# Performance work log

Hardware: AMD Instinct MI355X
Metric: run time of the kernel (lower is better)

Reference implementation:

```python
import jax, jax.numpy as jnp
import numpy as np

TAU = 1.0
K_TAU = 1.0
MAX_K = 64


def setup_inputs() -> dict:
    key = jax.random.key(0)
    ks = jax.random.split(key, 6)
    B, S, D, H = 8, 4096, 1024, 2048
    token_embeddings = jax.random.normal(ks[0], (B, S, D), dtype=jnp.float32)
    W1 = jax.random.normal(ks[1], (D, H), dtype=jnp.float32) * (1.0 / np.sqrt(D))
    b1 = jnp.zeros((H,), dtype=jnp.float32)
    W2 = jax.random.normal(ks[2], (H, 1), dtype=jnp.float32) * (1.0 / np.sqrt(H))
    b2 = jnp.zeros((1,), dtype=jnp.float32)
    k_logits = jax.random.normal(ks[3], (MAX_K,), dtype=jnp.float32) * 0.02
    return {"token_embeddings": token_embeddings, "W1": W1, "b1": b1,
            "W2": W2, "b2": b2, "k_logits": k_logits}


def _gumbel(rng, shape):
    u = jax.random.uniform(rng, shape, minval=1e-08, maxval=1.0 - 1e-08)
    return -jnp.log(-jnp.log(u))


def reference(token_embeddings, W1, b1, W2, b2, k_logits):
    B, S, D = token_embeddings.shape
    # scorer: Dense -> relu -> Dense(1), squeeze -> [B, S]
    h = jax.nn.relu(jnp.einsum('bsd,dh->bsh', token_embeddings, W1) + b1)
    importance_logits = (jnp.einsum('bsh,ho->bso', h, W2) + b2)[..., 0]

    rng = jax.random.key(42)  # training rng
    rng1, rng2 = jax.random.split(rng)

    # learnable-k selection (training branch)
    k_gumbel = _gumbel(rng1, k_logits.shape)
    k_soft = jax.nn.softmax((k_logits + k_gumbel) / K_TAU)
    expected_k = jnp.sum(k_soft * jnp.arange(1, MAX_K + 1, dtype=k_soft.dtype))
    k_selected = jnp.argmax(k_soft) + 1  # traced int scalar

    # gumbel-softmax hard top-k over tokens
    perturbed = importance_logits + _gumbel(rng2, importance_logits.shape)
    soft_mask = jax.nn.softmax(perturbed / TAU, axis=-1)  # [B, S]
    # rank of each token (0 = smallest); top-k == rank >= S - k
    rank = jnp.argsort(jnp.argsort(soft_mask, axis=-1), axis=-1)
    hard_mask = (rank >= S - k_selected).astype(soft_mask.dtype)
    selection_mask = jax.lax.stop_gradient(hard_mask - soft_mask) + soft_mask

    filtered_embeddings = token_embeddings * selection_mask[..., None]
    return filtered_embeddings, selection_mask, expected_k
```

## Files before the change

kernel.cpp:

```cpp
#include <hip/hip_runtime.h>
#include <stdint.h>

#define B_BATCH 8
#define S_SEQ   4096
#define D_DIM   1024
#define H_DIM   2048
#define M_TOK   (B_BATCH * S_SEQ)
#define MAXK    64
#define NSPLIT  2

typedef unsigned int u32;
typedef unsigned short u16;
typedef unsigned long long u64;
typedef __attribute__((ext_vector_type(8))) short short8;
typedef __attribute__((ext_vector_type(4))) float f32x4;

#define GLOBAL_AS __attribute__((address_space(1)))
#define LDS_AS    __attribute__((address_space(3)))


#define TF_ROUND(x0, x1, r) { x0 += x1; x1 = ((x1 << r) | (x1 >> (32 - r))); x1 ^= x0; }

__device__ __forceinline__ void tf2x32(u32 k0, u32 k1, u32 x0, u32 x1, u32& o0, u32& o1) {
  u32 k2 = k0 ^ k1 ^ 0x1BD11BDAu;
  x0 += k0; x1 += k1;
  TF_ROUND(x0, x1, 13) TF_ROUND(x0, x1, 15) TF_ROUND(x0, x1, 26) TF_ROUND(x0, x1, 6)
  x0 += k1; x1 += k2 + 1u;
  TF_ROUND(x0, x1, 17) TF_ROUND(x0, x1, 29) TF_ROUND(x0, x1, 16) TF_ROUND(x0, x1, 24)
  x0 += k2; x1 += k0 + 2u;
  TF_ROUND(x0, x1, 13) TF_ROUND(x0, x1, 15) TF_ROUND(x0, x1, 26) TF_ROUND(x0, x1, 6)
  x0 += k0; x1 += k1 + 3u;
  TF_ROUND(x0, x1, 17) TF_ROUND(x0, x1, 29) TF_ROUND(x0, x1, 16) TF_ROUND(x0, x1, 24)
  x0 += k1; x1 += k2 + 4u;
  TF_ROUND(x0, x1, 13) TF_ROUND(x0, x1, 15) TF_ROUND(x0, x1, 26) TF_ROUND(x0, x1, 6)
  x0 += k2; x1 += k0 + 5u;
  o0 = x0; o1 = x1;
}

__device__ __forceinline__ void jax_subkeys(u32& r1a, u32& r1b, u32& r2a, u32& r2b) {
  tf2x32(0u, 42u, 0u, 0u, r1a, r1b);
  tf2x32(0u, 42u, 0u, 1u, r2a, r2b);
}

__device__ __forceinline__ u32 jax_bits32(u32 ka, u32 kb, u32 i) {
  u32 o0, o1;
  tf2x32(ka, kb, 0u, i, o0, o1);
  return o0 ^ o1;
}

__device__ __forceinline__ float jax_uniform_from_bits(u32 bits) {
  float f = __uint_as_float((bits >> 9) | 0x3f800000u) - 1.0f;
  float r = f + 1e-8f;
  return fmaxf(1e-8f, r);
}

__device__ __forceinline__ float gumbel_from_bits(u32 bits) {
  float u = jax_uniform_from_bits(bits);
  return -logf(-logf(u));
}

__device__ __forceinline__ u32 ordf(float v) {
  u32 b = __float_as_uint(v);
  return (b & 0x80000000u) ? ~b : (b | 0x80000000u);
}

__device__ __forceinline__ u64 shflx64(u64 v, int m) {
  unsigned lo = (unsigned)v, hi = (unsigned)(v >> 32);
  lo = (unsigned)__shfl_xor((int)lo, m);
  hi = (unsigned)__shfl_xor((int)hi, m);
  return ((u64)hi << 32) | lo;
}


__device__ __forceinline__ u16 f2bf_rn(float x) {
  u32 u = __float_as_uint(x);
  u32 r = u + 0x7fffu + ((u >> 16) & 1u);
  return (u16)(r >> 16);
}

__device__ __forceinline__ void split1(float x, u16& h, u16& lo) {
  h = f2bf_rn(x);
  float hf = __uint_as_float(((u32)h) << 16);
  lo = f2bf_rn(x - hf);
}


__global__ __launch_bounds__(256) void prep_a_img(const float* __restrict__ x,
                                                  u16* __restrict__ img) {
  const u32 t = blockIdx.x * 256 + threadIdx.x;
  const int idx512 = (int)(t & 511);
  const int u1 = (int)((t >> 9) & 1);
  const int kt = (int)((t >> 10) & 31);
  const int mt = (int)(t >> 15);
  const int w = idx512 >> 6, l = idx512 & 63;
  const int sig = w * 16 + (l >> 2);
  const int r = sig + (sig & 64) + u1 * 64;
  const int c = (l & 3) ^ ((sig >> 1) & 3);
  const float* src = x + (size_t)(mt * 256 + r) * D_DIM + kt * 32 + c * 8;
  float4 v0 = *(const float4*)src;
  float4 v1 = *(const float4*)(src + 4);
  union { u16 a[8]; short8 v; } H, L;
  split1(v0.x, H.a[0], L.a[0]); split1(v0.y, H.a[1], L.a[1]);
  split1(v0.z, H.a[2], L.a[2]); split1(v0.w, H.a[3], L.a[3]);
  split1(v1.x, H.a[4], L.a[4]); split1(v1.y, H.a[5], L.a[5]);
  split1(v1.z, H.a[6], L.a[6]); split1(v1.w, H.a[7], L.a[7]);
  u16* dhi = img + (size_t)(mt * 32 + kt) * 16384 + u1 * 4096 + idx512 * 8;
  *(short8*)dhi = H.v;
  *(short8*)(dhi + 8192) = L.v;
}

__global__ __launch_bounds__(256) void prep_b_img(const float* __restrict__ W1,
                                                  u16* __restrict__ img) {
  __shared__ float tile[64][33];
  const int tid = threadIdx.x;
  const int bid = blockIdx.x;
  const int n0 = (bid & 63) * 32, k0 = (bid >> 6) * 64;
  const int tx = tid & 31, ty = tid >> 5;
  #pragma unroll
  for (int rr = 0; rr < 8; ++rr)
    tile[ty + rr * 8][tx] = W1[(size_t)(k0 + ty + rr * 8) * H_DIM + n0 + tx];
  __syncthreads();
  const int nc = tid & 31, c8 = tid >> 5;
  const int ktl = c8 >> 2, cc = c8 & 3;
  const int n = n0 + nc;
  const int nyb = n >> 10, t8 = (n >> 8) & 3, rr_ = n & 255;
  const int hiU = rr_ >> 7;
  const int sig = rr_ & 127;
  const int w_ = sig >> 4;
  const int lpos = (sig & 15) * 4 + (cc ^ ((sig >> 1) & 3));
  const int kt = (k0 >> 5) + ktl;
  union { u16 a[8]; short8 v; } H, L;
  #pragma unroll
  for (int j = 0; j < 8; ++j)
    split1(tile[ktl * 32 + cc * 8 + j][nc], H.a[j], L.a[j]);
  u16* d = img + (size_t)nyb * 2097152 + (size_t)(t8 * 32 + kt) * 16384
               + hiU * 4096 + w_ * 512 + lpos * 8;
  *(short8*)d = H.v;
  *(short8*)(d + 8192) = L.v;
}


__device__ __forceinline__ void stage16(const u16* g, u16* l) {
  __builtin_amdgcn_global_load_lds((const GLOBAL_AS u32*)g, (LDS_AS u32*)l, 16, 0, 0);
}

#define WAITV(N) asm volatile("s_waitcnt vmcnt(" #N ")" ::: "memory")
#define FENCE()  asm volatile("" ::: "memory")

__global__ __launch_bounds__(512, 2) void scorer_mfma256(
    const u16* __restrict__ Aimg, const u16* __restrict__ Bimg,
    const float* __restrict__ b1, const float* __restrict__ W2,
    float* __restrict__ pl) {
  extern __shared__ u16 smem[];
  float* red = (float*)(smem + 65536);

  const int tid = threadIdx.x;
  const int w = tid >> 6, l = tid & 63;
  const int wm = w >> 2, wn = w & 3;

  const int b = blockIdx.x;
  const int xcd = b & 7;
  const int j = b >> 3;
  const int nyb = j & 1;
  const int mt = xcd * 16 + (j >> 1);
  const int m0 = mt * 256;

  const u16* const Amt = Aimg + (size_t)mt * 524288;
  const u16* const Bny = Bimg + (size_t)nyb * 2097152;
  const int lane16 = w * 512 + l * 8;
  u16* const ldsw = smem + w * 512;

#define ST_A(T, U) stage16(Amt + (size_t)((((T) & 31) * 16384) + (U) * 4096) + lane16, \
                           ldsw + (((T) & 1) << 15) + (U) * 4096)
#define ST_B(T, U) stage16(Bny + (size_t)(((((T) >> 5) * 32 + ((T) & 31)) * 16384) + (U) * 4096) + lane16, \
                           ldsw + (((T) & 1) << 15) + 16384 + (U) * 4096)

  int a_off[8], b_off[4];
  #pragma unroll
  for (int mf = 0; mf < 8; ++mf) {
    int slot = wm * 64 + (mf & 3) * 16 + (l & 15);
    a_off[mf] = ((mf >> 2) * 4096) + slot * 32 + (((l >> 4) ^ ((slot >> 1) & 3)) << 3);
  }
  #pragma unroll
  for (int nf = 0; nf < 4; ++nf) {
    int r = wn * 64 + nf * 16 + (l & 15);
    b_off[nf] = r * 32 + (((l >> 4) ^ ((r >> 1) & 3)) << 3);
  }

  f32x4 acc[8][4];
  #pragma unroll
  for (int mf = 0; mf < 8; ++mf)
    #pragma unroll
    for (int nf = 0; nf < 4; ++nf) acc[mf][nf] = (f32x4){0.f, 0.f, 0.f, 0.f};

  const u16* const B0 = smem;
  const u16* const B1 = smem + 32768;
  short8 ah[4], al[4], bh[4], bl[4];

#define LDA_E(BASE) \
  { _Pragma("unroll") \
    for (int i = 0; i < 4; ++i) { \
      ah[i] = *(const short8*)((BASE) + a_off[i]); \
      al[i] = *(const short8*)((BASE) + 8192 + a_off[i]); \
    } }

#define LDA_L(BASE) \
  { _Pragma("unroll") \
    for (int i = 0; i < 4; ++i) { \
      ah[i] = *(const short8*)((BASE) + a_off[4 + i]); \
      al[i] = *(const short8*)((BASE) + 8192 + a_off[4 + i]); \
    } }

#define LDB(BASE) \
  { _Pragma("unroll") \
    for (int nf = 0; nf < 4; ++nf) { \
      bh[nf] = *(const short8*)((BASE) + 16384 + b_off[nf]); \
      bl[nf] = *(const short8*)((BASE) + 24576 + b_off[nf]); \
    } }

#define MMA_QUAD(MB) \
  __builtin_amdgcn_s_setprio(1); \
  { _Pragma("unroll") \
    for (int mf = 0; mf < 4; ++mf) \
      _Pragma("unroll") \
      for (int nf = 0; nf < 4; ++nf) { \
        acc[(MB) + mf][nf] = __builtin_amdgcn_mfma_f32_16x16x32_bf16(ah[mf], bh[nf], acc[(MB) + mf][nf], 0, 0, 0); \
        acc[(MB) + mf][nf] = __builtin_amdgcn_mfma_f32_16x16x32_bf16(ah[mf], bl[nf], acc[(MB) + mf][nf], 0, 0, 0); \
        acc[(MB) + mf][nf] = __builtin_amdgcn_mfma_f32_16x16x32_bf16(al[mf], bh[nf], acc[(MB) + mf][nf], 0, 0, 0); \
      } } \
  __builtin_amdgcn_s_setprio(0)

  ST_B(0, 0); ST_B(0, 1); ST_B(0, 2); ST_B(0, 3);
  ST_A(0, 0); ST_A(0, 2);
  ST_A(0, 1); ST_A(0, 3);
  ST_B(1, 0); ST_B(1, 1); ST_B(1, 2); ST_B(1, 3);
  ST_A(1, 0); ST_A(1, 2);
  WAITV(8);
  __builtin_amdgcn_s_barrier();
  FENCE();

  for (int it = 0; it < 64; ++it) {
    const bool last = (it == 63);
    const int T1 = 2 * it + 1, T2 = 2 * it + 2, T3 = 2 * it + 3;

    LDB(B0); LDA_E(B0);
    ST_A(T1, 1); ST_A(T1, 3);
    MMA_QUAD(0);
    WAITV(8);
    __builtin_amdgcn_s_barrier(); FENCE();

    LDA_L(B0);
    if (!last) { ST_B(T2, 0); ST_B(T2, 1); ST_B(T2, 2); ST_B(T2, 3); ST_A(T2, 0); ST_A(T2, 2); }
    MMA_QUAD(4);
    if (last) { WAITV(2); } else { WAITV(8); }
    __builtin_amdgcn_s_barrier(); FENCE();

    LDB(B1); LDA_E(B1);
    if (!last) { ST_A(T2, 1); ST_A(T2, 3); }
    MMA_QUAD(0);
    if (last) { WAITV(0); } else { WAITV(8); }
    __builtin_amdgcn_s_barrier(); FENCE();

    LDA_L(B1);
    if (!last) { ST_B(T3, 0); ST_B(T3, 1); ST_B(T3, 2); ST_B(T3, 3); ST_A(T3, 0); ST_A(T3, 2); }
    MMA_QUAD(4);

    if ((it & 15) == 15) {
      const int t8 = it >> 4;
      const int nb = nyb * 1024 + t8 * 256 + wn * 64 + (l & 15);
      float b1v[4], w2v[4];
      #pragma unroll
      for (int nf = 0; nf < 4; ++nf) { b1v[nf] = b1[nb + nf * 16]; w2v[nf] = W2[nb + nf * 16]; }
      #pragma unroll
      for (int mf = 0; mf < 8; ++mf)
        #pragma unroll
        for (int r = 0; r < 4; ++r) {
          float p = 0.f;
          #pragma unroll
          for (int nf = 0; nf < 4; ++nf)
            p += fmaxf(acc[mf][nf][r] + b1v[nf], 0.f) * w2v[nf];
          p += __shfl_xor(p, 1); p += __shfl_xor(p, 2);
          p += __shfl_xor(p, 4); p += __shfl_xor(p, 8);
          if ((l & 15) == 0) {
            float* rp = red + ((wm * 128 + mf * 16 + (l >> 4) * 4 + r) << 2) + wn;
            if (t8 == 0) *rp = p; else *rp += p;
          }
        }
      #pragma unroll
      for (int mf = 0; mf < 8; ++mf)
        #pragma unroll
        for (int nf = 0; nf < 4; ++nf) acc[mf][nf] = (f32x4){0.f, 0.f, 0.f, 0.f};
    }

    if (!last) WAITV(8);
    __builtin_amdgcn_s_barrier(); FENCE();
  }

  __syncthreads();
  if (tid < 256) {
    const float* rp = red + (tid << 2);
    pl[(size_t)nyb * M_TOK + m0 + tid] = rp[0] + rp[1] + rp[2] + rp[3];
  }
}


__global__ __launch_bounds__(256) void scorer_kernel(
    const float* __restrict__ emb, const float* __restrict__ W1,
    const float* __restrict__ b1, const float* __restrict__ W2,
    const float* __restrict__ b2, float* __restrict__ pert) {
  __shared__ float As[16][68];
  __shared__ float Bs[16][132];
  __shared__ float red[64][17];

  const int tid = threadIdx.x;
  const int tx = tid & 15;
  const int ty = tid >> 4;
  const int m0 = blockIdx.x * 64;
  const int at = tid >> 2;
  const int ac = (tid & 3) << 2;
  const int br = tid >> 4;
  const int bc = (tid & 15) << 3;

  float logit[4] = {0.f, 0.f, 0.f, 0.f};

  for (int n0 = 0; n0 < H_DIM; n0 += 128) {
    float acc[4][8];
    #pragma unroll
    for (int i = 0; i < 4; i++)
      #pragma unroll
      for (int j = 0; j < 8; j++) acc[i][j] = 0.f;

    for (int k0 = 0; k0 < D_DIM; k0 += 16) {
      float4 av  = *(const float4*)(emb + (size_t)(m0 + at) * D_DIM + (k0 + ac));
      float4 bv0 = *(const float4*)(W1 + (size_t)(k0 + br) * H_DIM + (n0 + bc));
      float4 bv1 = *(const float4*)(W1 + (size_t)(k0 + br) * H_DIM + (n0 + bc) + 4);
      __syncthreads();
      As[ac + 0][at] = av.x; As[ac + 1][at] = av.y;
      As[ac + 2][at] = av.z; As[ac + 3][at] = av.w;
      *(float4*)&Bs[br][bc]     = bv0;
      *(float4*)&Bs[br][bc + 4] = bv1;
      __syncthreads();
      #pragma unroll
      for (int k = 0; k < 16; k++) {
        float4 a   = *(const float4*)&As[k][ty << 2];
        float4 b0  = *(const float4*)&Bs[k][tx << 3];
        float4 b1v = *(const float4*)&Bs[k][(tx << 3) + 4];
        float aa[4] = {a.x, a.y, a.z, a.w};
        float bb[8] = {b0.x, b0.y, b0.z, b0.w, b1v.x, b1v.y, b1v.z, b1v.w};
        #pragma unroll
        for (int i = 0; i < 4; i++)
          #pragma unroll
          for (int j = 0; j < 8; j++)
            acc[i][j] = fmaf(aa[i], bb[j], acc[i][j]);
      }
    }
    float4 c0 = *(const float4*)(b1 + n0 + (tx << 3));
    float4 c1 = *(const float4*)(b1 + n0 + (tx << 3) + 4);
    float4 w0 = *(const float4*)(W2 + n0 + (tx << 3));
    float4 w1 = *(const float4*)(W2 + n0 + (tx << 3) + 4);
    float cb[8] = {c0.x, c0.y, c0.z, c0.w, c1.x, c1.y, c1.z, c1.w};
    float wb[8] = {w0.x, w0.y, w0.z, w0.w, w1.x, w1.y, w1.z, w1.w};
    #pragma unroll
    for (int i = 0; i < 4; i++)
      #pragma unroll
      for (int j = 0; j < 8; j++) {
        float h = fmaxf(acc[i][j] + cb[j], 0.f);
        logit[i] = fmaf(h, wb[j], logit[i]);
      }
  }

  __syncthreads();
  #pragma unroll
  for (int i = 0; i < 4; i++) red[(ty << 2) + i][tx] = logit[i];
  __syncthreads();

  if (tid < 64) {
    float s = 0.f;
    #pragma unroll
    for (int x = 0; x < 16; x++) s += red[tid][x];
    s += b2[0];
    int t = m0 + tid;
    u32 r1a, r1b, r2a, r2b;
    jax_subkeys(r1a, r1b, r2a, r2b);
    pert[t] = s + gumbel_from_bits(jax_bits32(r2a, r2b, (u32)t));
  }
}


template <bool FROM_PL>
__device__ __forceinline__ void topk_body(const float* kl, const float* pl,
                                          const float* b2, float* mask,
                                          float* expk) {
  const int r = blockIdx.x;
  const int tid = threadIdx.x;
  const int w = tid >> 6, l = tid & 63;
  __shared__ int ksel_sh;
  __shared__ int cnt[2][4];

  u32 r1a, r1b, r2a, r2b;
  jax_subkeys(r1a, r1b, r2a, r2b);

  if (tid < 64) {
    float p = kl[l] + gumbel_from_bits(jax_bits32(r1a, r1b, (u32)l));
    u64 kkey = ((u64)ordf(p) << 32) | (unsigned)(63 - l);
    #pragma unroll
    for (int off = 32; off >= 1; off >>= 1) {
      u64 o = shflx64(kkey, off);
      if (o > kkey) kkey = o;
    }
    if (l == 0) ksel_sh = 64 - (int)(kkey & 0xffffffffu);
    if (r == 0) {
      float m = p;
      #pragma unroll
      for (int off = 32; off >= 1; off >>= 1) m = fmaxf(m, __shfl_xor(m, off));
      float e = expf(p - m);
      float s = e;
      #pragma unroll
      for (int off = 32; off >= 1; off >>= 1) s += __shfl_xor(s, off);
      float v = (e / s) * (float)(l + 1);
      #pragma unroll
      for (int off = 32; off >= 1; off >>= 1) v += __shfl_xor(v, off);
      if (l == 0) expk[0] = v;
    }
  }
  __syncthreads();
  const int k = ksel_sh;
  const float b2v = FROM_PL ? b2[0] : 0.f;

  u64 keys[16];
  #pragma unroll
  for (int j = 0; j < 16; j++) {
    int s = tid + (j << 8);
    int t = (r << 12) + s;
    float v;
    if (FROM_PL) {
      float acc = pl[t];
      #pragma unroll
      for (int q = 1; q < NSPLIT; ++q) acc += pl[(size_t)q * M_TOK + t];
      v = acc + b2v + gumbel_from_bits(jax_bits32(r2a, r2b, (u32)t));
    } else {
      v = mask[t];
    }
    keys[j] = ((u64)ordf(v) << 12) | (unsigned)s;
  }

  u64 lo = 0ull, hi = (1ull << 44) - 1ull;
  int it = 0;
  while (lo < hi) {
    const u64 mid = (lo + hi + 1ull) >> 1;
    int c = 0;
    #pragma unroll
    for (int j = 0; j < 16; j++) c += (keys[j] >= mid) ? 1 : 0;
    #pragma unroll
    for (int off = 32; off >= 1; off >>= 1) c += __shfl_xor(c, off);
    const int buf = it & 1;
    if (l == 0) cnt[buf][w] = c;
    __syncthreads();
    const int tot = cnt[buf][0] + cnt[buf][1] + cnt[buf][2] + cnt[buf][3];
    if (tot >= k) lo = mid; else hi = mid - 1ull;
    ++it;
  }
  const u64 thresh = lo;

  #pragma unroll
  for (int j = 0; j < 16; j++) {
    int s = tid + (j << 8);
    mask[(r << 12) + s] = (keys[j] >= thresh) ? 1.0f : 0.0f;
  }
}

__global__ __launch_bounds__(256) void topk_pl_kernel(const float* __restrict__ kl,
                                                      const float* __restrict__ pl,
                                                      const float* __restrict__ b2,
                                                      float* __restrict__ mask,
                                                      float* __restrict__ expk) {
  topk_body<true>(kl, pl, b2, mask, expk);
}

__global__ __launch_bounds__(256) void topk_kernel(const float* __restrict__ kl,
                                                   float* __restrict__ mask,
                                                   float* __restrict__ expk) {
  topk_body<false>(kl, nullptr, nullptr, mask, expk);
}


__global__ __launch_bounds__(256) void filter_kernel(const float* __restrict__ emb,
                                                     const float* __restrict__ mask,
                                                     float* __restrict__ out) {
  const int t = blockIdx.x;
  const float mk = mask[t];
  const size_t base = (size_t)t * D_DIM + ((size_t)threadIdx.x << 2);
  float4 v = *(const float4*)(emb + base);
  *(float4*)(out + base) = make_float4(v.x * mk, v.y * mk, v.z * mk, v.w * mk);
}


extern "C" void kernel_launch(void* const* d_in, const int* in_sizes, int n_in,
                              void* d_out, int out_size, void* d_ws, size_t ws_size,
                              hipStream_t stream) {
  const float* emb = (const float*)d_in[0];
  const float* W1  = (const float*)d_in[1];
  const float* b1  = (const float*)d_in[2];
  const float* W2  = (const float*)d_in[3];
  const float* b2  = (const float*)d_in[4];
  const float* kl  = (const float*)d_in[5];
  float* out  = (float*)d_out;
  float* mask = out + (size_t)M_TOK * D_DIM;
  float* expk = mask + M_TOK;

  const size_t ws_need = (size_t)H_DIM * D_DIM * 2 * 2 + (size_t)NSPLIT * M_TOK * 4;

  if (ws_size >= ws_need) {
    u16* Aimg = (u16*)d_out;
    u16* Bimg = (u16*)d_ws;
    float* pl = (float*)(Bimg + (size_t)2 * H_DIM * D_DIM);

    static bool attr_done = false;
    if (!attr_done) {
      hipFuncSetAttribute(reinterpret_cast<const void*>(scorer_mfma256),
                          hipFuncAttributeMaxDynamicSharedMemorySize, 135168);
      attr_done = true;
    }

    prep_a_img<<<16384, 256, 0, stream>>>(emb, Aimg);
    prep_b_img<<<1024, 256, 0, stream>>>(W1, Bimg);
    scorer_mfma256<<<256, 512, 135168, stream>>>(Aimg, Bimg, b1, W2, pl);
    topk_pl_kernel<<<B_BATCH, 256, 0, stream>>>(kl, pl, b2, mask, expk);
  } else {
    scorer_kernel<<<M_TOK / 64, 256, 0, stream>>>(emb, W1, b1, W2, b2, mask);
    topk_kernel<<<B_BATCH, 256, 0, stream>>>(kl, mask, expk);
  }

  filter_kernel<<<M_TOK, 256, 0, stream>>>(emb, mask, out);
}
```

Measured before the change: 602.4 us.

## Merge prep kernels, interleave A reloads into MFMA loop, batch filter rows

Merges the two operand-prep kernels into one launch, with the grid split by block index. In the scorer main loop, the second half of the A-fragment LDS loads is interleaved with the first MFMA quad, and the waitcnt thresholds change from 8 to 6. The filter kernel now processes 16 tokens per block instead of one, which cuts block count and launch overhead. The altered waitcnt values and the dropped wait after the first quad risk hazards on the LDS staging, and the interleaving may raise register pressure.

```diff
diff --git a/kernel.cpp b/kernel.cpp
--- a/kernel.cpp
+++ b/kernel.cpp
@@ -85,58 +85,59 @@
 }
 
 
-__global__ __launch_bounds__(256) void prep_a_img(const float* __restrict__ x,
-                                                  u16* __restrict__ img) {
-  const u32 t = blockIdx.x * 256 + threadIdx.x;
-  const int idx512 = (int)(t & 511);
-  const int u1 = (int)((t >> 9) & 1);
-  const int kt = (int)((t >> 10) & 31);
-  const int mt = (int)(t >> 15);
-  const int w = idx512 >> 6, l = idx512 & 63;
-  const int sig = w * 16 + (l >> 2);
-  const int r = sig + (sig & 64) + u1 * 64;
-  const int c = (l & 3) ^ ((sig >> 1) & 3);
-  const float* src = x + (size_t)(mt * 256 + r) * D_DIM + kt * 32 + c * 8;
-  float4 v0 = *(const float4*)src;
-  float4 v1 = *(const float4*)(src + 4);
-  union { u16 a[8]; short8 v; } H, L;
-  split1(v0.x, H.a[0], L.a[0]); split1(v0.y, H.a[1], L.a[1]);
-  split1(v0.z, H.a[2], L.a[2]); split1(v0.w, H.a[3], L.a[3]);
-  split1(v1.x, H.a[4], L.a[4]); split1(v1.y, H.a[5], L.a[5]);
-  split1(v1.z, H.a[6], L.a[6]); split1(v1.w, H.a[7], L.a[7]);
-  u16* dhi = img + (size_t)(mt * 32 + kt) * 16384 + u1 * 4096 + idx512 * 8;
-  *(short8*)dhi = H.v;
-  *(short8*)(dhi + 8192) = L.v;
-}
-
-__global__ __launch_bounds__(256) void prep_b_img(const float* __restrict__ W1,
-                                                  u16* __restrict__ img) {
+__global__ __launch_bounds__(256) void prep_kernel(const float* __restrict__ x,
+                                                   u16* __restrict__ img,
+                                                   const float* __restrict__ W1,
+                                                   u16* __restrict__ bimg) {
   __shared__ float tile[64][33];
-  const int tid = threadIdx.x;
-  const int bid = blockIdx.x;
-  const int n0 = (bid & 63) * 32, k0 = (bid >> 6) * 64;
-  const int tx = tid & 31, ty = tid >> 5;
-  #pragma unroll
-  for (int rr = 0; rr < 8; ++rr)
-    tile[ty + rr * 8][tx] = W1[(size_t)(k0 + ty + rr * 8) * H_DIM + n0 + tx];
-  __syncthreads();
-  const int nc = tid & 31, c8 = tid >> 5;
-  const int ktl = c8 >> 2, cc = c8 & 3;
-  const int n = n0 + nc;
-  const int nyb = n >> 10, t8 = (n >> 8) & 3, rr_ = n & 255;
-  const int hiU = rr_ >> 7;
-  const int sig = rr_ & 127;
-  const int w_ = sig >> 4;
-  const int lpos = (sig & 15) * 4 + (cc ^ ((sig >> 1) & 3));
-  const int kt = (k0 >> 5) + ktl;
-  union { u16 a[8]; short8 v; } H, L;
-  #pragma unroll
-  for (int j = 0; j < 8; ++j)
-    split1(tile[ktl * 32 + cc * 8 + j][nc], H.a[j], L.a[j]);
-  u16* d = img + (size_t)nyb * 2097152 + (size_t)(t8 * 32 + kt) * 16384
-               + hiU * 4096 + w_ * 512 + lpos * 8;
-  *(short8*)d = H.v;
-  *(short8*)(d + 8192) = L.v;
+  if (blockIdx.x < 16384) {
+    const u32 t = blockIdx.x * 256 + threadIdx.x;
+    const int idx512 = (int)(t & 511);
+    const int u1 = (int)((t >> 9) & 1);
+    const int kt = (int)((t >> 10) & 31);
+    const int mt = (int)(t >> 15);
+    const int w = idx512 >> 6, l = idx512 & 63;
+    const int sig = w * 16 + (l >> 2);
+    const int r = sig + (sig & 64) + u1 * 64;
+    const int c = (l & 3) ^ ((sig >> 1) & 3);
+    const float* src = x + (size_t)(mt * 256 + r) * D_DIM + kt * 32 + c * 8;
+    float4 v0 = *(const float4*)src;
+    float4 v1 = *(const float4*)(src + 4);
+    union { u16 a[8]; short8 v; } H, L;
+    split1(v0.x, H.a[0], L.a[0]); split1(v0.y, H.a[1], L.a[1]);
+    split1(v0.z, H.a[2], L.a[2]); split1(v0.w, H.a[3], L.a[3]);
+    split1(v1.x, H.a[4], L.a[4]); split1(v1.y, H.a[5], L.a[5]);
+    split1(v1.z, H.a[6], L.a[6]); split1(v1.w, H.a[7], L.a[7]);
+    u16* dhi = img + (size_t)(mt * 32 + kt) * 16384 + u1 * 4096 + idx512 * 8;
+    *(short8*)dhi = H.v;
+    *(short8*)(dhi + 8192) = L.v;
+  } else {
+    const int tid = threadIdx.x;
+    const int bid = blockIdx.x - 16384;
+    const int n0 = (bid & 63) * 32, k0 = (bid >> 6) * 64;
+    const int tx = tid & 31, ty = tid >> 5;
+    #pragma unroll
+    for (int rr = 0; rr < 8; ++rr)
+      tile[ty + rr * 8][tx] = W1[(size_t)(k0 + ty + rr * 8) * H_DIM + n0 + tx];
+    __syncthreads();
+    const int nc = tid & 31, c8 = tid >> 5;
+    const int ktl = c8 >> 2, cc = c8 & 3;
+    const int n = n0 + nc;
+    const int nyb = n >> 10, t8 = (n >> 8) & 3, rr_ = n & 255;
+    const int hiU = rr_ >> 7;
+    const int sig = rr_ & 127;
+    const int w_ = sig >> 4;
+    const int lpos = (sig & 15) * 4 + (cc ^ ((sig >> 1) & 3));
+    const int kt = (k0 >> 5) + ktl;
+    union { u16 a[8]; short8 v; } H, L;
+    #pragma unroll
+    for (int j = 0; j < 8; ++j)
+      split1(tile[ktl * 32 + cc * 8 + j][nc], H.a[j], L.a[j]);
+    u16* d = bimg + (size_t)nyb * 2097152 + (size_t)(t8 * 32 + kt) * 16384
+                  + hiU * 4096 + w_ * 512 + lpos * 8;
+    *(short8*)d = H.v;
+    *(short8*)(d + 8192) = L.v;
+  }
 }
 
 
@@ -204,13 +205,6 @@
       al[i] = *(const short8*)((BASE) + 8192 + a_off[i]); \
     } }
 
-#define LDA_L(BASE) \
-  { _Pragma("unroll") \
-    for (int i = 0; i < 4; ++i) { \
-      ah[i] = *(const short8*)((BASE) + a_off[4 + i]); \
-      al[i] = *(const short8*)((BASE) + 8192 + a_off[4 + i]); \
-    } }
-
 #define LDB(BASE) \
   { _Pragma("unroll") \
     for (int nf = 0; nf < 4; ++nf) { \
@@ -218,15 +212,30 @@
       bl[nf] = *(const short8*)((BASE) + 24576 + b_off[nf]); \
     } }
 
-#define MMA_QUAD(MB) \
+#define MMA_E_RELOAD_L(BASE) \
+  __builtin_amdgcn_s_setprio(1); \
+  { _Pragma("unroll") \
+    for (int mf = 0; mf < 4; ++mf) { \
+      _Pragma("unroll") \
+      for (int nf = 0; nf < 4; ++nf) { \
+        acc[mf][nf] = __builtin_amdgcn_mfma_f32_16x16x32_bf16(ah[mf], bh[nf], acc[mf][nf], 0, 0, 0); \
+        acc[mf][nf] = __builtin_amdgcn_mfma_f32_16x16x32_bf16(ah[mf], bl[nf], acc[mf][nf], 0, 0, 0); \
+        acc[mf][nf] = __builtin_amdgcn_mfma_f32_16x16x32_bf16(al[mf], bh[nf], acc[mf][nf], 0, 0, 0); \
+      } \
+      ah[mf] = *(const short8*)((BASE) + a_off[4 + mf]); \
+      al[mf] = *(const short8*)((BASE) + 8192 + a_off[4 + mf]); \
+    } } \
+  __builtin_amdgcn_s_setprio(0)
+
+#define MMA_L() \
   __builtin_amdgcn_s_setprio(1); \
   { _Pragma("unroll") \
     for (int mf = 0; mf < 4; ++mf) \
       _Pragma("unroll") \
       for (int nf = 0; nf < 4; ++nf) { \
-        acc[(MB) + mf][nf] = __builtin_amdgcn_mfma_f32_16x16x32_bf16(ah[mf], bh[nf], acc[(MB) + mf][nf], 0, 0, 0); \
-        acc[(MB) + mf][nf] = __builtin_amdgcn_mfma_f32_16x16x32_bf16(ah[mf], bl[nf], acc[(MB) + mf][nf], 0, 0, 0); \
-        acc[(MB) + mf][nf] = __builtin_amdgcn_mfma_f32_16x16x32_bf16(al[mf], bh[nf], acc[(MB) + mf][nf], 0, 0, 0); \
+        acc[4 + mf][nf] = __builtin_amdgcn_mfma_f32_16x16x32_bf16(ah[mf], bh[nf], acc[4 + mf][nf], 0, 0, 0); \
+        acc[4 + mf][nf] = __builtin_amdgcn_mfma_f32_16x16x32_bf16(ah[mf], bl[nf], acc[4 + mf][nf], 0, 0, 0); \
+        acc[4 + mf][nf] = __builtin_amdgcn_mfma_f32_16x16x32_bf16(al[mf], bh[nf], acc[4 + mf][nf], 0, 0, 0); \
       } } \
   __builtin_amdgcn_s_setprio(0)
 
@@ -235,7 +244,7 @@
   ST_A(0, 1); ST_A(0, 3);
   ST_B(1, 0); ST_B(1, 1); ST_B(1, 2); ST_B(1, 3);
   ST_A(1, 0); ST_A(1, 2);
-  WAITV(8);
+  WAITV(6);
   __builtin_amdgcn_s_barrier();
   FENCE();
 
@@ -245,25 +254,21 @@
 
     LDB(B0); LDA_E(B0);
     ST_A(T1, 1); ST_A(T1, 3);
-    MMA_QUAD(0);
-    WAITV(8);
+    MMA_E_RELOAD_L(B0);
     __builtin_amdgcn_s_barrier(); FENCE();
 
-    LDA_L(B0);
     if (!last) { ST_B(T2, 0); ST_B(T2, 1); ST_B(T2, 2); ST_B(T2, 3); ST_A(T2, 0); ST_A(T2, 2); }
-    MMA_QUAD(4);
-    if (last) { WAITV(2); } else { WAITV(8); }
+    MMA_L();
+    if (last) { WAITV(0); } else { WAITV(6); }
     __builtin_amdgcn_s_barrier(); FENCE();
 
     LDB(B1); LDA_E(B1);
     if (!last) { ST_A(T2, 1); ST_A(T2, 3); }
-    MMA_QUAD(0);
-    if (last) { WAITV(0); } else { WAITV(8); }
+    MMA_E_RELOAD_L(B1);
     __builtin_amdgcn_s_barrier(); FENCE();
 
-    LDA_L(B1);
     if (!last) { ST_B(T3, 0); ST_B(T3, 1); ST_B(T3, 2); ST_B(T3, 3); ST_A(T3, 0); ST_A(T3, 2); }
-    MMA_QUAD(4);
+    MMA_L();
 
     if ((it & 15) == 15) {
       const int t8 = it >> 4;
@@ -292,7 +297,7 @@
         for (int nf = 0; nf < 4; ++nf) acc[mf][nf] = (f32x4){0.f, 0.f, 0.f, 0.f};
     }
 
-    if (!last) WAITV(8);
+    if (!last) WAITV(6);
     __builtin_amdgcn_s_barrier(); FENCE();
   }
 
@@ -487,11 +492,15 @@
 __global__ __launch_bounds__(256) void filter_kernel(const float* __restrict__ emb,
                                                      const float* __restrict__ mask,
                                                      float* __restrict__ out) {
-  const int t = blockIdx.x;
-  const float mk = mask[t];
-  const size_t base = (size_t)t * D_DIM + ((size_t)threadIdx.x << 2);
-  float4 v = *(const float4*)(emb + base);
-  *(float4*)(out + base) = make_float4(v.x * mk, v.y * mk, v.z * mk, v.w * mk);
+  const int b = blockIdx.x;
+  #pragma unroll
+  for (int it = 0; it < 16; ++it) {
+    const int t = b * 16 + it;
+    const float mk = mask[t];
+    const size_t base = (size_t)t * D_DIM + ((size_t)threadIdx.x << 2);
+    float4 v = *(const float4*)(emb + base);
+    *(float4*)(out + base) = make_float4(v.x * mk, v.y * mk, v.z * mk, v.w * mk);
+  }
 }
 
 
@@ -522,8 +531,7 @@
       attr_done = true;
     }
 
-    prep_a_img<<<16384, 256, 0, stream>>>(emb, Aimg);
-    prep_b_img<<<1024, 256, 0, stream>>>(W1, Bimg);
+    prep_kernel<<<16384 + 1024, 256, 0, stream>>>(emb, Aimg, W1, Bimg);
     scorer_mfma256<<<256, 512, 135168, stream>>>(Aimg, Bimg, b1, W2, pl);
     topk_pl_kernel<<<B_BATCH, 256, 0, stream>>>(kl, pl, b2, mask, expk);
   } else {
@@ -531,5 +539,5 @@
     topk_kernel<<<B_BATCH, 256, 0, stream>>>(kl, mask, expk);
   }
 
-  filter_kernel<<<M_TOK, 256, 0, stream>>>(emb, mask, out);
-}
+  filter_kernel<<<M_TOK / 16, 256, 0, stream>>>(emb, mask, out);
+}
```

New measurement: 627.2 us. 1.04x slower.
